# Optimization experiments

Measured on AMD Instinct MI355X. Metric: run time of the kernel, lower is better.

The kernel has to match this reference:

```python
import jax, jax.numpy as jnp
import numpy as np

D_K = 128  # d_model / h


def setup_inputs() -> dict:
    key = jax.random.key(0)
    ks = jax.random.split(key, 7)
    N, d_model, h, d_k = 8192, 2048, 16, D_K
    q = jax.random.normal(ks[0], (N, d_model), dtype=jnp.float32)
    # per-head projection weights, RandomNormal(stddev=1.0) in source
    Wq = jax.random.normal(ks[1], (h, d_model, d_k), dtype=jnp.float32)
    Wk = jax.random.normal(ks[2], (h, d_model, d_k), dtype=jnp.float32)
    Wv = jax.random.normal(ks[3], (h, d_model, d_k), dtype=jnp.float32)
    # learned key/value rows and output proj, keras 'uniform' init (+-0.05)
    k_param = jax.random.uniform(ks[4], (1, d_model), dtype=jnp.float32, minval=-0.05, maxval=0.05)
    v_param = jax.random.uniform(ks[5], (1, d_model), dtype=jnp.float32, minval=-0.05, maxval=0.05)
    Wo = jax.random.uniform(ks[6], (d_model, d_model), dtype=jnp.float32, minval=-0.05, maxval=0.05)
    return {"q": q, "Wq": Wq, "Wk": Wk, "Wv": Wv, "k_param": k_param, "v_param": v_param, "Wo": Wo}


def reference(q, Wq, Wk, Wv, k_param, v_param, Wo):
    d_k = Wq.shape[-1]
    scale = jnp.sqrt(jnp.float32(d_k))
    # batched per-head projections: (h, N, d_k), (h, 1, d_k)
    q_proj = jnp.einsum('nd,hdk->hnk', q, Wq)
    k_proj = jnp.einsum('od,hdk->hok', k_param, Wk)
    v_proj = jnp.einsum('od,hdk->hok', v_param, Wv)
    scores = jnp.einsum('hnk,hok->hno', q_proj, k_proj) / scale  # (h, N, 1)
    weights = jax.nn.softmax(scores, axis=-1)  # size-1 softmax -> ones (faithful)
    head_out = jnp.einsum('hno,hok->hnk', weights, v_proj)  # (h, N, d_k)
    N = q.shape[0]
    concat = jnp.transpose(head_out, (1, 0, 2)).reshape(N, -1)  # (N, h*d_k)
    return concat @ Wo
```

## Files before the change

### kernel.cpp

```cpp
#include <hip/hip_runtime.h>


#define DM 2048
#define H  16
#define DK 128

__device__ __forceinline__ void fma4(float4& a, float s, const float4& w) {
    a.x += s * w.x; a.y += s * w.y; a.z += s * w.z; a.w += s * w.w;
}

__global__ __launch_bounds__(256) void k_vp(const float* __restrict__ Wv,
                                            const float* __restrict__ vparam,
                                            float* __restrict__ part1,
                                            float* __restrict__ r) {
    const int b  = blockIdx.x;
    const int t  = threadIdx.x;
    const int h  = b & 15;
    const int ds = b >> 4;
    const int k4 = t & 31;
    const int dg = t >> 5;
    const int d0 = ds * 64 + dg * 8;

    const float* base = Wv + ((size_t)h * DM + d0) * DK + 4 * k4;
    float4 acc = {0.f, 0.f, 0.f, 0.f};
#pragma unroll
    for (int i = 0; i < 8; ++i) {
        const float4 w4 = *(const float4*)(base + (size_t)i * DK);
        fma4(acc, vparam[d0 + i], w4);
    }

    __shared__ float4 sred[8][32];
    sred[dg][k4] = acc;
    __syncthreads();
    if (t < 32) {
        float4 s = sred[0][t];
#pragma unroll
        for (int g = 1; g < 8; ++g) {
            const float4 v = sred[g][t];
            s.x += v.x; s.y += v.y; s.z += v.z; s.w += v.w;
        }
        *(float4*)(part1 + (size_t)ds * DM + h * DK + 4 * t) = s;
    }

    if (b < 8) r[(b << 8) + t] = 0.f;
}

__global__ __launch_bounds__(256) void k_gemv(const float* __restrict__ part1,
                                              const float* __restrict__ Wo,
                                              float* __restrict__ r) {
    const int ms = blockIdx.x;
    const int jq = blockIdx.y;
    const int t  = threadIdx.x;

    __shared__ float vph[2][128];
    __shared__ float vp_s[128];
    {
        const int jl = t & 127;
        const int hf = t >> 7;
        const float* p = part1 + (size_t)(hf * 16) * DM + jq * 128 + jl;
        float s = 0.f;
#pragma unroll
        for (int c = 0; c < 16; ++c) s += p[(size_t)c * DM];
        vph[hf][jl] = s;
    }
    __syncthreads();
    if (t < 128) vp_s[t] = vph[0][t] + vph[1][t];
    __syncthreads();

    const int m4 = t & 15;
    const int jg = t >> 4;
    const float* wo = Wo + (size_t)(jq * 128 + jg * 8) * DM + ms * 64 + 4 * m4;
    float4 acc = {0.f, 0.f, 0.f, 0.f};
#pragma unroll
    for (int i = 0; i < 8; ++i) {
        const float4 w4 = *(const float4*)(wo + (size_t)i * DM);
        fma4(acc, vp_s[jg * 8 + i], w4);
    }

    __shared__ float4 red4[16][16];
    red4[jg][m4] = acc;
    __syncthreads();
    if (t < 64) {
        const int mm = t & 15;
        const int cc = t >> 4;
        float s = 0.f;
#pragma unroll
        for (int g = 0; g < 16; ++g) s += ((const float*)&red4[g][mm])[cc];
        atomicAdd(&r[ms * 64 + 4 * mm + cc], s);
    }
}

__global__ __launch_bounds__(256) void k_bcast(const float* __restrict__ r,
                                               float* __restrict__ out) {
    const int b = blockIdx.x;
    const int t = threadIdx.x;
    const float4 v0 = ((const float4*)r)[t];
    const float4 v1 = ((const float4*)r)[256 + t];
    float4* o4 = (float4*)out + (size_t)b * 16 * (DM / 4);
#pragma unroll
    for (int n = 0; n < 16; ++n) {
        o4[(size_t)n * (DM / 4) + t]       = v0;
        o4[(size_t)n * (DM / 4) + 256 + t] = v1;
    }
}

extern "C" void kernel_launch(void* const* d_in, const int* in_sizes, int n_in,
                              void* d_out, int out_size, void* d_ws, size_t ws_size,
                              hipStream_t stream) {
    const float* Wv     = (const float*)d_in[3];
    const float* vparam = (const float*)d_in[5];
    const float* Wo     = (const float*)d_in[6];
    float* out = (float*)d_out;

    float* part1 = (float*)d_ws;
    float* r     = part1 + 32 * DM;

    k_vp   <<<512,          256, 0, stream>>>(Wv, vparam, part1, r);
    k_gemv <<<dim3(32, 16), 256, 0, stream>>>(part1, Wo, r);
    k_bcast<<<512,          256, 0, stream>>>(r, out);
}
```

Baseline: 26.31 us.

## Fuse v-projection and Wo GEMV into one kernel with per-head counter sync

Result: slower. 63.15 us (+140.1%).

```diff
diff --git a/kernel.cpp b/kernel.cpp
--- a/kernel.cpp
+++ b/kernel.cpp
@@ -1,56 +1,98 @@
 #include <hip/hip_runtime.h>
 
 
-#define DM 2048
-#define H  16
-#define DK 128
+#define DM     2048
+#define H      16
+#define DK     128
+#define POISON 0xAAAAAAAAu
+#define TARGET 40u
 
 __device__ __forceinline__ void fma4(float4& a, float s, const float4& w) {
     a.x += s * w.x; a.y += s * w.y; a.z += s * w.z; a.w += s * w.w;
 }
+__device__ __forceinline__ float ld_coh(const float* p) {
+    return __hip_atomic_load(p, __ATOMIC_RELAXED, __HIP_MEMORY_SCOPE_AGENT);
+}
+__device__ __forceinline__ void st_coh(float* p, float v) {
+    __hip_atomic_store(p, v, __ATOMIC_RELAXED, __HIP_MEMORY_SCOPE_AGENT);
+}
 
-__global__ __launch_bounds__(256) void k_vp(const float* __restrict__ Wv,
-                                            const float* __restrict__ vparam,
-                                            float* __restrict__ part1,
-                                            float* __restrict__ r) {
-    const int b  = blockIdx.x;
-    const int t  = threadIdx.x;
+__global__ __launch_bounds__(256, 2) void k12(
+    const float* __restrict__ Wv,
+    const float* __restrict__ vparam,
+    const float* __restrict__ Wo,
+    float* __restrict__ part1,
+    float* __restrict__ r,
+    unsigned int* __restrict__ done)
+{
+    const int b = blockIdx.x;
+    const int t = threadIdx.x;
+
+    if (t < 16) {
+        atomicCAS(&done[t], POISON, 0u);
+        atomicCAS(&done[t], TARGET, 0u);
+    }
+
     const int h  = b & 15;
     const int ds = b >> 4;
     const int k4 = t & 31;
     const int dg = t >> 5;
     const int d0 = ds * 64 + dg * 8;
+    {
+        const float* base = Wv + ((size_t)h * DM + d0) * DK + 4 * k4;
+        float4 acc = {0.f, 0.f, 0.f, 0.f};
+#pragma unroll
+        for (int i = 0; i < 8; ++i)
+            fma4(acc, vparam[d0 + i], *(const float4*)(base + (size_t)i * DK));
+        __shared__ float4 sred[8][32];
+        sred[dg][k4] = acc;
+        __syncthreads();
+        if (t < 32) {
+            float4 s = sred[0][t];
+#pragma unroll
+            for (int g = 1; g < 8; ++g) {
+                const float4 v = sred[g][t];
+                s.x += v.x; s.y += v.y; s.z += v.z; s.w += v.w;
+            }
+            float* dst = part1 + (size_t)ds * DM + h * DK + 4 * t;
+            st_coh(dst + 0, s.x); st_coh(dst + 1, s.y);
+            st_coh(dst + 2, s.z); st_coh(dst + 3, s.w);
+        }
+    }
+    if (b < 8) st_coh(&r[(b << 8) + t], 0.f);
 
-    const float* base = Wv + ((size_t)h * DM + d0) * DK + 4 * k4;
-    float4 acc = {0.f, 0.f, 0.f, 0.f};
+    __syncthreads();
+    if (t == 0) {
+        __hip_atomic_fetch_add(&done[h], 1u, __ATOMIC_RELAXED,
+                               __HIP_MEMORY_SCOPE_AGENT);
+        if (b < 8)
 #pragma unroll
-    for (int i = 0; i < 8; ++i) {
-        const float4 w4 = *(const float4*)(base + (size_t)i * DK);
-        fma4(acc, vparam[d0 + i], w4);
+            for (int i = 0; i < 16; ++i)
+                __hip_atomic_fetch_add(&done[i], 1u, __ATOMIC_RELAXED,
+                                       __HIP_MEMORY_SCOPE_AGENT);
     }
 
-    __shared__ float4 sred[8][32];
-    sred[dg][k4] = acc;
-    __syncthreads();
-    if (t < 32) {
-        float4 s = sred[0][t];
+    const int ms = b & 31;
+    const int jq = b >> 5;
+    const int m4 = t & 15;
+    const int jg = t >> 4;
+    float4 w[8];
+    {
+        const float* wop = Wo + (size_t)(jq * 128 + jg * 8) * DM + ms * 64 + 4 * m4;
 #pragma unroll
-        for (int g = 1; g < 8; ++g) {
-            const float4 v = sred[g][t];
-            s.x += v.x; s.y += v.y; s.z += v.z; s.w += v.w;
-        }
-        *(float4*)(part1 + (size_t)ds * DM + h * DK + 4 * t) = s;
+        for (int i = 0; i < 8; ++i) w[i] = *(const float4*)(wop + (size_t)i * DM);
     }
 
-    if (b < 8) r[(b << 8) + t] = 0.f;
-}
-
-__global__ __launch_bounds__(256) void k_gemv(const float* __restrict__ part1,
-                                              const float* __restrict__ Wo,
-                                              float* __restrict__ r) {
-    const int ms = blockIdx.x;
-    const int jq = blockIdx.y;
-    const int t  = threadIdx.x;
+    if (t == 0) {
+        int it = 0;
+        do {
+            unsigned v = __hip_atomic_fetch_add(&done[jq], 0u, __ATOMIC_RELAXED,
+                                                __HIP_MEMORY_SCOPE_AGENT);
+            if (v >= TARGET) break;
+            __builtin_amdgcn_s_sleep(64);
+        } while (++it < (1 << 16));
+    }
+    __syncthreads();
 
     __shared__ float vph[2][128];
     __shared__ float vp_s[128];
@@ -60,25 +102,18 @@
         const float* p = part1 + (size_t)(hf * 16) * DM + jq * 128 + jl;
         float s = 0.f;
 #pragma unroll
-        for (int c = 0; c < 16; ++c) s += p[(size_t)c * DM];
+        for (int c = 0; c < 16; ++c) s += ld_coh(&p[(size_t)c * DM]);
         vph[hf][jl] = s;
     }
     __syncthreads();
     if (t < 128) vp_s[t] = vph[0][t] + vph[1][t];
     __syncthreads();
 
-    const int m4 = t & 15;
-    const int jg = t >> 4;
-    const float* wo = Wo + (size_t)(jq * 128 + jg * 8) * DM + ms * 64 + 4 * m4;
-    float4 acc = {0.f, 0.f, 0.f, 0.f};
+    float4 a2 = {0.f, 0.f, 0.f, 0.f};
 #pragma unroll
-    for (int i = 0; i < 8; ++i) {
-        const float4 w4 = *(const float4*)(wo + (size_t)i * DM);
-        fma4(acc, vp_s[jg * 8 + i], w4);
-    }
-
+    for (int i = 0; i < 8; ++i) fma4(a2, vp_s[jg * 8 + i], w[i]);
     __shared__ float4 red4[16][16];
-    red4[jg][m4] = acc;
+    red4[jg][m4] = a2;
     __syncthreads();
     if (t < 64) {
         const int mm = t & 15;
@@ -112,10 +147,10 @@
     const float* Wo     = (const float*)d_in[6];
     float* out = (float*)d_out;
 
-    float* part1 = (float*)d_ws;
-    float* r     = part1 + 32 * DM;
+    float* part1       = (float*)d_ws;
+    float* r           = part1 + 32 * DM;
+    unsigned int* done = (unsigned int*)(r + DM);
 
-    k_vp   <<<512,          256, 0, stream>>>(Wv, vparam, part1, r);
-    k_gemv <<<dim3(32, 16), 256, 0, stream>>>(part1, Wo, r);
-    k_bcast<<<512,          256, 0, stream>>>(r, out);
+    k12    <<<512, 256, 0, stream>>>(Wv, vparam, Wo, part1, r, done);
+    k_bcast<<<512, 256, 0, stream>>>(r, out);
 }
```
